# Kernel tuning notes

Hardware: AMD Instinct MI355X
Metric: run time of the kernel (lower is better)

Reference implementation:

```python
import jax, jax.numpy as jnp
import numpy as np

B, T, H, OUT_LEN, D_IN, D_OUT = 512, 512, 256, 8, 64, 64

def _lstm_seq(x, Wih, Whh, bih, bhh):
    # batch_first LSTM, zero initial state; x: [B,T,D] -> [B,T,H]
    b = bih + bhh
    h0 = jnp.zeros((x.shape[0], Whh.shape[1]), x.dtype)
    def step(carry, xt):
        h, c = carry
        g = xt @ Wih.T + h @ Whh.T + b
        i, f, gg, o = jnp.split(g, 4, axis=-1)  # torch gate order i,f,g,o
        c = jax.nn.sigmoid(f) * c + jax.nn.sigmoid(i) * jnp.tanh(gg)
        h = jax.nn.sigmoid(o) * jnp.tanh(c)
        return (h, c), h
    _, hs = jax.lax.scan(step, (h0, h0), jnp.swapaxes(x, 0, 1))
    return jnp.swapaxes(hs, 0, 1)

def _lstm_cell0(xt, Wih, bih, bhh):
    # single decode step; original calls self.dec with fresh zero (h,c) each
    # step, so the recurrent matrix Whh never contributes.
    g = xt @ Wih.T + bih + bhh
    i, f, gg, o = jnp.split(g, 4, axis=-1)
    c = jax.nn.sigmoid(i) * jnp.tanh(gg)
    return jax.nn.sigmoid(o) * jnp.tanh(c)

def _mlp(x, Ws, bs, Wl, bl):
    # simple.mlp: hidden Linear+ReLU stack, linear output (dropout off)
    for k in range(Ws.shape[0]):
        x = jax.nn.relu(x @ Ws[k] + bs[k])
    return x @ Wl + bl

def setup_inputs():
    key = jax.random.key(0)
    ks = iter(jax.random.split(key, 32))
    def W(shape, fan):
        return jax.random.normal(next(ks), shape, jnp.float32) / np.float32(np.sqrt(fan))
    return {
        'x': jax.random.normal(next(ks), (B, T, D_IN), jnp.float32),
        'in_W': W((D_IN, H), D_IN), 'in_b': jnp.zeros((H,), jnp.float32),
        'enc_Wih': W((4*H, H), H), 'enc_Whh': W((4*H, H), H),
        'enc_bih': jnp.zeros((4*H,), jnp.float32), 'enc_bhh': jnp.zeros((4*H,), jnp.float32),
        'dec_Wih': W((4*H, 2*H), 2*H), 'dec_Whh': W((4*H, H), H),
        'dec_bih': jnp.zeros((4*H,), jnp.float32), 'dec_bhh': jnp.zeros((4*H,), jnp.float32),
        'w_Ws': W((3, H, H), H), 'w_bs': jnp.zeros((3, H), jnp.float32), 'w_Wl': W((H, H), H), 'w_bl': jnp.zeros((H,), jnp.float32),
        'u_Ws': W((3, H, H), H), 'u_bs': jnp.zeros((3, H), jnp.float32), 'u_Wl': W((H, H), H), 'u_bl': jnp.zeros((H,), jnp.float32),
        'v_Ws': W((7, H, H), H), 'v_bs': jnp.zeros((7, H), jnp.float32), 'v_Wl': W((H, 1), H), 'v_bl': jnp.zeros((1,), jnp.float32),
        'out_W': W((H, D_OUT), H), 'out_b': jnp.zeros((D_OUT,), jnp.float32),
    }

def reference(x, in_W, in_b, enc_Wih, enc_Whh, enc_bih, enc_bhh,
              dec_Wih, dec_Whh, dec_bih, dec_bhh,
              w_Ws, w_bs, w_Wl, w_bl, u_Ws, u_bs, u_Wl, u_bl,
              v_Ws, v_bs, v_Wl, v_bl, out_W, out_b):
    h = x @ in_W + in_b                                       # input projection [B,T,H]
    enc = _lstm_seq(h, enc_Wih, enc_Whh, enc_bih, enc_bhh)    # [B,T,H]
    whs = _mlp(enc, w_Ws, w_bs, w_Wl, w_bl)                   # w(hs), loop-invariant (hoisted)
    def dec_step(s, _):
        us = _mlp(s, u_Ws, u_bs, u_Wl, u_bl)                  # [B,H]
        e = _mlp(jnp.tanh(us[:, None, :] + whs), v_Ws, v_bs, v_Wl, v_bl)  # [B,T,1]
        a = jax.nn.softmax(e, axis=1)                         # softmax over time
        c_t = jnp.sum(a * enc, axis=1)                        # [B,H] weighted sum
        s_new = _lstm_cell0(jnp.concatenate([c_t, s], axis=-1), dec_Wih, dec_bih, dec_bhh)
        return s_new, s_new
    s0 = jnp.zeros((x.shape[0], H), x.dtype)
    _, ss = jax.lax.scan(dec_step, s0, None, length=OUT_LEN)  # [OUT_LEN,B,H]
    dec = jnp.swapaxes(ss, 0, 1)                              # [B,OUT_LEN,H]
    return dec @ out_W + out_b                                # output projection
```

## Files before the change

kernel.cpp:

```cpp
#include <hip/hip_runtime.h>
#include <math.h>

#define B_    512
#define T_    512
#define H_    256
#define DIN_  64
#define OL_   8
#define DOUT_ 64

#define CBv   128
#define HSTR  32768

typedef unsigned short u16;
typedef unsigned int u32;
typedef unsigned long long ull;
typedef __attribute__((ext_vector_type(8))) short short8;
typedef __attribute__((ext_vector_type(4))) float f32x4;

static __device__ __forceinline__ float sigm(float x){ return 1.0f/(1.0f + expf(-x)); }
static __device__ __forceinline__ float bf2f(u16 h){
  u32 u = ((u32)h) << 16; float f; __builtin_memcpy(&f, &u, 4); return f;
}
static __device__ __forceinline__ u16 f2bf(float f){
  u32 u; __builtin_memcpy(&u, &f, 4);
  u = (u + 0x7fffu + ((u >> 16) & 1u)) >> 16;
  return (u16)u;
}
static __device__ __forceinline__ u32 packhl(float f){
  u16 h = f2bf(f);
  u16 lo = f2bf(f - bf2f(h));
  return ((u32)h << 16) | (u32)lo;
}
static __device__ __forceinline__ float unpackhl(u32 w){
  return bf2f((u16)(w >> 16)) + bf2f((u16)(w & 0xffff));
}
static __device__ __forceinline__ u32 al(const u32* p){
  return __hip_atomic_load(p, __ATOMIC_RELAXED, __HIP_MEMORY_SCOPE_AGENT);
}
static __device__ __forceinline__ void as_(u32* p, u32 v){
  __hip_atomic_store(p, v, __ATOMIC_RELAXED, __HIP_MEMORY_SCOPE_AGENT);
}

__global__ void k_wpt(const float* __restrict__ inW, const float* __restrict__ Wih,
                      float* __restrict__ WpT)
{
  int gid = blockIdx.x * 256 + threadIdx.x;
  int c = gid >> 6, d = gid & 63;
  const float* wr = Wih + c * H_;
  const float* ir = inW + d * H_;
  float acc = 0.f;
  #pragma unroll 4
  for (int e = 0; e < H_; e += 4) {
    float4 av = *(const float4*)(ir + e);
    float4 bv = *(const float4*)(wr + e);
    acc += av.x*bv.x + av.y*bv.y + av.z*bv.z + av.w*bv.w;
  }
  WpT[c*64 + d] = acc;
}

__global__ void k_bp(const float* __restrict__ inb, const float* __restrict__ Wih,
                     const float* __restrict__ bih, const float* __restrict__ bhh,
                     float* __restrict__ bp)
{
  int c = blockIdx.x * 256 + threadIdx.x;
  const float* wr = Wih + c * H_;
  float acc = bih[c] + bhh[c];
  for (int e = 0; e < H_; ++e) acc += inb[e] * wr[e];
  bp[c] = acc;
}

__global__ void k_dwt(const float* __restrict__ dWih, float* __restrict__ dWt)
{
  int gid = blockIdx.x * 256 + threadIdx.x;
  int j = gid >> 9, k = gid & 511;
  int row = (j < 256) ? j : (j + 256);
  dWt[k*768 + j] = dWih[row*512 + k];
}

__global__ void k_wall(const float* __restrict__ wWs, const float* __restrict__ wWl,
                       const float* __restrict__ uWs, const float* __restrict__ uWl,
                       const float* __restrict__ vWs, u16* __restrict__ outb)
{
  int lyr = blockIdx.y;
  const float* W = (lyr < 3)  ? wWs + lyr*65536
                 : (lyr == 3) ? wWl
                 : (lyr < 7)  ? uWs + (lyr-4)*65536
                 : (lyr == 7) ? uWl
                 :              vWs + (lyr-8)*65536;
  u16* out = outb + (size_t)lyr*131072;
  int gid = blockIdx.x * 256 + threadIdx.x;
  int k = gid & 255, n = gid >> 8;
  float v = W[k*256 + n];
  int s = k >> 5, j = k & 7;
  int lane = (((k >> 3) & 3) << 4) | (n & 15);
  int fl = ((s*16) + (n >> 4))*512 + lane*8 + j;
  u16 h = f2bf(v);
  out[fl] = h;
  out[65536 + fl] = f2bf(v - bf2f(h));
}

__global__ void k_whhfl(const float* __restrict__ Whh, u16* __restrict__ out)
{
  int gid = blockIdx.x * 256 + threadIdx.x;
  int j = gid & 7, l = (gid >> 3) & 63, ctg = (gid >> 9) & 63, s = gid >> 15;
  int k = s*32 + (l >> 4)*8 + j;
  int wv = ctg >> 2, g = ctg & 3;
  int row = g*256 + wv*16 + (l & 15);
  float v = Whh[row*256 + k];
  int fl = (s*64 + ctg)*512 + l*8 + j;
  u16 h = f2bf(v);
  out[fl] = h;
  out[262144 + fl] = f2bf(v - bf2f(h));
}

__global__ void k_wpfl(const float* __restrict__ WpT, u16* __restrict__ out)
{
  int gid = blockIdx.x * 256 + threadIdx.x;
  int j = gid & 7, l = (gid >> 3) & 63, ctg = (gid >> 9) & 63, s = gid >> 15;
  int k = s*32 + (l >> 4)*8 + j;
  int wv = ctg >> 2, g = ctg & 3;
  int row = g*256 + wv*16 + (l & 15);
  float v = WpT[row*64 + k];
  int fl = (s*64 + ctg)*512 + l*8 + j;
  u16 h = f2bf(v);
  out[fl] = h;
  out[65536 + fl] = f2bf(v - bf2f(h));
}

__global__ __launch_bounds__(256,1) void k_enc(
    const float* __restrict__ x, const u16* __restrict__ whhFL,
    const u16* __restrict__ wpFL, const float* __restrict__ bp,
    u32* __restrict__ henc)
{
  __shared__ float G[2][16][32][4];
  const int tid = threadIdx.x, l = tid & 63, wv = tid >> 6;
  const int lr = l & 15, lk = l >> 4;
  const int rg = blockIdx.x, bg = blockIdx.y, z = blockIdx.z;
  const int ug2 = wv >> 1;
  const int g0 = (wv & 1) * 2;
  const int u16g = bg*2 + ug2;

  short8 whH[8][2], whL[8][2], wpH[2][2], wpL[2][2];
  #pragma unroll
  for (int s = 0; s < 8; ++s)
    #pragma unroll
    for (int c = 0; c < 2; ++c) {
      int ctg = u16g*4 + g0 + c;
      whH[s][c] = *(const short8*)(whhFL + ((size_t)(s*64 + ctg))*512 + l*8);
      whL[s][c] = *(const short8*)(whhFL + 262144 + ((size_t)(s*64 + ctg))*512 + l*8);
    }
  #pragma unroll
  for (int s = 0; s < 2; ++s)
    #pragma unroll
    for (int c = 0; c < 2; ++c) {
      int ctg = u16g*4 + g0 + c;
      wpH[s][c] = *(const short8*)(wpFL + ((size_t)(s*64 + ctg))*512 + l*8);
      wpL[s][c] = *(const short8*)(wpFL + 65536 + ((size_t)(s*64 + ctg))*512 + l*8);
    }
  const int ul = tid & 31, er0 = tid >> 5;
  float bb[4];
  #pragma unroll
  for (int g = 0; g < 4; ++g) bb[g] = bp[g*256 + bg*32 + ul];
  float cs[2] = {0.f, 0.f};

  u32* hz = henc + (size_t)z * (size_t)(T_+1) * HSTR;
  const float* xrow = x + ((size_t)(z*CBv + rg*16 + lr)*T_)*DIN_ + lk*8;

  for (int t = 0; t < T_; ++t) {
    float4 xv0 = *(const float4*)(xrow);
    float4 xv1 = *(const float4*)(xrow + 4);
    float4 xv2 = *(const float4*)(xrow + 32);
    float4 xv3 = *(const float4*)(xrow + 36);
    xrow += DIN_;

    const ull* hb = (const ull*)(hz + (size_t)t*HSTR + (size_t)(rg*16 + lr)*256);
    ull hq[8][4];
    #pragma unroll
    for (int s = 0; s < 8; ++s)
      #pragma unroll
      for (int q = 0; q < 4; ++q)
        hq[s][q] = __hip_atomic_load(hb + s*16 + lk*4 + q,
                                     __ATOMIC_RELAXED, __HIP_MEMORY_SCOPE_AGENT);
    if (t) {
      for (;;) {
        bool ok = true;
        #pragma unroll
        for (int s = 0; s < 8; ++s)
          #pragma unroll
          for (int q = 0; q < 4; ++q) {
            u32 a = (u32)hq[s][q], b = (u32)(hq[s][q] >> 32);
            ok = ok && (a != 0u) && (b != 0u);
          }
        if (__all(ok)) break;
        __builtin_amdgcn_s_sleep(1);
        #pragma unroll
        for (int s = 0; s < 8; ++s)
          #pragma unroll
          for (int q = 0; q < 4; ++q)
            hq[s][q] = __hip_atomic_load(hb + s*16 + lk*4 + q,
                                         __ATOMIC_RELAXED, __HIP_MEMORY_SCOPE_AGENT);
      }
    }

    f32x4 acc[2];
    acc[0] = (f32x4){0.f,0.f,0.f,0.f};
    acc[1] = (f32x4){0.f,0.f,0.f,0.f};

    #pragma unroll
    for (int s = 0; s < 2; ++s) {
      float vv[8];
      if (s == 0) { vv[0]=xv0.x;vv[1]=xv0.y;vv[2]=xv0.z;vv[3]=xv0.w;vv[4]=xv1.x;vv[5]=xv1.y;vv[6]=xv1.z;vv[7]=xv1.w; }
      else        { vv[0]=xv2.x;vv[1]=xv2.y;vv[2]=xv2.z;vv[3]=xv2.w;vv[4]=xv3.x;vv[5]=xv3.y;vv[6]=xv3.z;vv[7]=xv3.w; }
      short8 ah, al2;
      #pragma unroll
      for (int j = 0; j < 8; ++j) {
        u16 h = f2bf(vv[j]);
        ah[j] = (short)h;
        al2[j] = (short)f2bf(vv[j] - bf2f(h));
      }
      #pragma unroll
      for (int c = 0; c < 2; ++c) {
        acc[c] = __builtin_amdgcn_mfma_f32_16x16x32_bf16(ah,  wpH[s][c], acc[c], 0,0,0);
        acc[c] = __builtin_amdgcn_mfma_f32_16x16x32_bf16(al2, wpH[s][c], acc[c], 0,0,0);
        acc[c] = __builtin_amdgcn_mfma_f32_16x16x32_bf16(ah,  wpL[s][c], acc[c], 0,0,0);
      }
    }
    #pragma unroll
    for (int s = 0; s < 8; ++s) {
      short8 ah, al2;
      #pragma unroll
      for (int q = 0; q < 4; ++q) {
        u32 w0 = (u32)hq[s][q], w1 = (u32)(hq[s][q] >> 32);
        ah[q*2]   = (short)(w0 >> 16); al2[q*2]   = (short)(w0 & 0xffff);
        ah[q*2+1] = (short)(w1 >> 16); al2[q*2+1] = (short)(w1 & 0xffff);
      }
      #pragma unroll
      for (int c = 0; c < 2; ++c) {
        acc[c] = __builtin_amdgcn_mfma_f32_16x16x32_bf16(ah,  whH[s][c], acc[c], 0,0,0);
        acc[c] = __builtin_amdgcn_mfma_f32_16x16x32_bf16(al2, whH[s][c], acc[c], 0,0,0);
        acc[c] = __builtin_amdgcn_mfma_f32_16x16x32_bf16(ah,  whL[s][c], acc[c], 0,0,0);
      }
    }

    const int p = t & 1;
    #pragma unroll
    for (int c = 0; c < 2; ++c)
      #pragma unroll
      for (int j = 0; j < 4; ++j)
        G[p][lk*4 + j][ug2*16 + lr][g0 + c] = acc[c][j];
    __syncthreads();

    #pragma unroll
    for (int pp = 0; pp < 2; ++pp) {
      int row = er0 + pp*8;
      float4 gq = *(const float4*)&G[p][row][ul][0];
      float gi = gq.x + bb[0], gf = gq.y + bb[1];
      float gg = gq.z + bb[2], go = gq.w + bb[3];
      float cn = sigm(gf)*cs[pp] + sigm(gi)*tanhf(gg);
      float hn = sigm(go)*tanhf(cn);
      cs[pp] = cn;
      as_(hz + (size_t)(t+1)*HSTR + (size_t)(rg*16 + row)*256 + bg*32 + ul,
          packhl(hn) | 1u);
    }
  }
}

static __device__ __forceinline__ void mlp_core(
    u32* act, const u16* wFL, const float* bs, const float* bl,
    int L, int nbs, bool lastRelu, int tid)
{
  const int l = tid & 63, cg = tid >> 6;
  const int lr = l & 15, lk = l >> 4;
  f32x4 acc[4][4];
  for (int lyr = 0; lyr < L; ++lyr) {
    __syncthreads();
    const u16* wb = wFL + (size_t)lyr*131072;
    #pragma unroll
    for (int rt = 0; rt < 4; ++rt)
      #pragma unroll
      for (int ct = 0; ct < 4; ++ct) acc[rt][ct] = (f32x4){0.f,0.f,0.f,0.f};

    short8 bh[2][4], blo[2][4];
    #pragma unroll
    for (int ct = 0; ct < 4; ++ct) {
      const u16* bfp = wb + ((size_t)(cg*4 + ct))*512 + l*8;
      bh[0][ct]  = *(const short8*)bfp;
      blo[0][ct] = *(const short8*)(bfp + 65536);
    }
    #pragma unroll
    for (int s = 0; s < 8; ++s) {
      const int pb = s & 1, nb = pb ^ 1;
      if (s < 7) {
        #pragma unroll
        for (int ct = 0; ct < 4; ++ct) {
          const u16* bfp = wb + ((size_t)((s+1)*16 + cg*4 + ct))*512 + l*8;
          bh[nb][ct]  = *(const short8*)bfp;
          blo[nb][ct] = *(const short8*)(bfp + 65536);
        }
      }
      short8 ah[4], al2[4];
      #pragma unroll
      for (int rt = 0; rt < 4; ++rt) {
        int row = rt*16 + lr;
        int cc = s*8 + lk*2;
        const u32* base = act + row*256;
        uint4 d0 = *(const uint4*)(base + (((cc    ) ^ (row & 7)) << 2));
        uint4 d1 = *(const uint4*)(base + (((cc + 1) ^ (row & 7)) << 2));
        u32 q[8] = {d0.x,d0.y,d0.z,d0.w,d1.x,d1.y,d1.z,d1.w};
        #pragma unroll
        for (int j = 0; j < 8; ++j) {
          ah[rt][j]  = (short)(q[j] >> 16);
          al2[rt][j] = (short)(q[j] & 0xffff);
        }
      }
      #pragma unroll
      for (int ct = 0; ct < 4; ++ct)
        #pragma unroll
        for (int rt = 0; rt < 4; ++rt) {
          acc[rt][ct] = __builtin_amdgcn_mfma_f32_16x16x32_bf16(ah[rt],  bh[pb][ct],  acc[rt][ct], 0,0,0);
          acc[rt][ct] = __builtin_amdgcn_mfma_f32_16x16x32_bf16(al2[rt], bh[pb][ct],  acc[rt][ct], 0,0,0);
          acc[rt][ct] = __builtin_amdgcn_mfma_f32_16x16x32_bf16(ah[rt],  blo[pb][ct], acc[rt][ct], 0,0,0);
        }
    }
    const float* bptr = (lyr < nbs) ? (bs + lyr*256) : bl;
    const bool dorelu = (lyr < L-1) || lastRelu;
    #pragma unroll
    for (int ct = 0; ct < 4; ++ct) {
      float bv = bptr[cg*64 + ct*16 + lr];
      #pragma unroll
      for (int rt = 0; rt < 4; ++rt)
        #pragma unroll
        for (int g = 0; g < 4; ++g) {
          float xv = acc[rt][ct][g] + bv;
          acc[rt][ct][g] = dorelu ? fmaxf(xv, 0.f) : xv;
        }
    }
    __syncthreads();
    #pragma unroll
    for (int ct = 0; ct < 4; ++ct) {
      int n = cg*64 + ct*16 + lr;
      #pragma unroll
      for (int rt = 0; rt < 4; ++rt)
        #pragma unroll
        for (int g = 0; g < 4; ++g) {
          int row = rt*16 + lk*4 + g;
          act[row*256 + (((n >> 2) ^ (row & 7)) << 2) + (n & 3)] = packhl(acc[rt][ct][g]);
        }
    }
  }
  __syncthreads();
}

__global__ __launch_bounds__(256,1) void k_dec_all(
    const u32* __restrict__ henc, const u16* __restrict__ mlpFL,
    const float* __restrict__ wbs, const float* __restrict__ wbl,
    const float* __restrict__ ubs, const float* __restrict__ ubl,
    const float* __restrict__ vbs, const float* __restrict__ vWl,
    const float* __restrict__ vbl,
    const float* __restrict__ dWt, const float* __restrict__ dbih,
    const float* __restrict__ dbhh,
    const float* __restrict__ oW, const float* __restrict__ ob,
    u32* __restrict__ whsP, u32* __restrict__ usb, u32* __restrict__ usflag,
    u32* __restrict__ eS, u32* __restrict__ ctxS, u32* __restrict__ sS,
    float* __restrict__ outc)
{
  extern __shared__ u32 act[];
  __shared__ float red[8];
  const int bid = blockIdx.x, tid = threadIdx.x;
  const u16* wFLw = mlpFL;
  const u16* wFLu = mlpFL + 4*131072;
  const u16* wFLv = mlpFL + 8*131072;
  float sprev[4] = {0.f, 0.f, 0.f, 0.f};

  for (int k = 0; k < 4; ++k) {
    long m0t = (long)(bid + 256*k) * 64;
    __syncthreads();
    for (int i = tid; i < 4096; i += 256) {
      int row = i >> 6, c16 = i & 63;
      long m = m0t + row;
      uint4 pk = *(const uint4*)(henc + HSTR + m*256 + c16*4);
      *((uint4*)(act + row*256 + ((c16 ^ (row & 7)) << 2))) = pk;
    }
    mlp_core(act, wFLw, wbs, wbl, 4, 3, false, tid);
    for (int i = tid; i < 4096; i += 256) {
      int row = i >> 6, c16 = i & 63;
      long m = m0t + row;
      uint4 pk = *((const uint4*)(act + row*256 + ((c16 ^ (row & 7)) << 2)));
      *(uint4*)(whsP + m*256 + c16*4) = pk;
    }
  }

  for (int s = 0; s < OL_; ++s) {
    if (bid < 2) {
      long m0t = (long)bid * 64;
      __syncthreads();
      for (int i = tid; i < 4096; i += 256) {
        int row = i >> 6, c16 = i & 63;
        const u32* sp = sS + (size_t)s*32768 + (m0t + row)*256 + c16*4;
        u32 w0 = al(sp), w1 = al(sp+1), w2 = al(sp+2), w3 = al(sp+3);
        if (s) {
          while (!(w0 && w1 && w2 && w3)) {
            __builtin_amdgcn_s_sleep(1);
            w0 = al(sp); w1 = al(sp+1); w2 = al(sp+2); w3 = al(sp+3);
          }
        }
        uint4 pk = { packhl(__uint_as_float(w0)), packhl(__uint_as_float(w1)),
                     packhl(__uint_as_float(w2)), packhl(__uint_as_float(w3)) };
        *((uint4*)(act + row*256 + ((c16 ^ (row & 7)) << 2))) = pk;
      }
      mlp_core(act, wFLu, ubs, ubl, 4, 3, false, tid);
      for (int i = tid; i < 4096; i += 256) {
        int row = i >> 6, c16 = i & 63;
        uint4 pk = *((const uint4*)(act + row*256 + ((c16 ^ (row & 7)) << 2)));
        *(uint4*)(usb + (size_t)s*32768 + (m0t + row)*256 + c16*4) = pk;
      }
      __syncthreads();
      if (tid == 0)
        __hip_atomic_store(usflag + s*2 + bid, 1u,
                           __ATOMIC_RELEASE, __HIP_MEMORY_SCOPE_AGENT);
    }

    {
      const u32* f0 = usflag + s*2;
      for (;;) {
        u32 a0 = al(f0), a1 = al(f0 + 1);
        if (a0 & a1) break;
        __builtin_amdgcn_s_sleep(2);
      }
      __builtin_amdgcn_fence(__ATOMIC_ACQUIRE, "agent");
    }

    for (int k = 0; k < 4; ++k) {
      long m0t = (long)(bid + 256*k) * 64;
      __syncthreads();
      for (int i = tid; i < 4096; i += 256) {
        int row = i >> 6, c16 = i & 63;
        long m = m0t + row;
        uint4 pw = *(const uint4*)(whsP + m*256 + c16*4);
        uint4 uw = *(const uint4*)(usb + (size_t)s*32768 + (m & 127)*256 + c16*4);
        uint4 pk;
        pk.x = packhl(tanhf(unpackhl(pw.x) + unpackhl(uw.x)));
        pk.y = packhl(tanhf(unpackhl(pw.y) + unpackhl(uw.y)));
        pk.z = packhl(tanhf(unpackhl(pw.z) + unpackhl(uw.z)));
        pk.w = packhl(tanhf(unpackhl(pw.w) + unpackhl(uw.w)));
        *((uint4*)(act + row*256 + ((c16 ^ (row & 7)) << 2))) = pk;
      }
      mlp_core(act, wFLv, vbs, vbs, 7, 7, true, tid);
      {
        int r2 = tid >> 2, q = tid & 3;
        float p = 0.f;
        #pragma unroll 8
        for (int j = 0; j < 64; ++j) {
          int n = q*64 + j;
          u32 w = act[r2*256 + (((n >> 2) ^ (r2 & 7)) << 2) + (n & 3)];
          p += unpackhl(w) * vWl[n];
        }
        p += __shfl_xor(p, 1, 64);
        p += __shfl_xor(p, 2, 64);
        if (q == 0)
          as_(eS + (size_t)s*65536 + m0t + r2, __float_as_uint(p + vbl[0]) | 1u);
      }
    }

    if (bid >= 64 && bid < 192) {
      int b = bid - 64;
      __syncthreads();
      float* asx = (float*)act;
      const u32* ep0 = eS + (size_t)s*65536 + b;
      u32 w0, w1;
      for (;;) {
        w0 = al(ep0 + (size_t)tid*128);
        w1 = al(ep0 + (size_t)(tid + 256)*128);
        if (w0 && w1) break;
        __builtin_amdgcn_s_sleep(1);
      }
      float v0 = __uint_as_float(w0), v1 = __uint_as_float(w1);
      const int lane = tid & 63, wv = tid >> 6;
      float m = fmaxf(v0, v1);
      #pragma unroll
      for (int o = 32; o; o >>= 1) m = fmaxf(m, __shfl_xor(m, o, 64));
      if (!lane) red[wv] = m;
      __syncthreads();
      m = fmaxf(fmaxf(red[0], red[1]), fmaxf(red[2], red[3]));
      float x0 = expf(v0 - m), x1 = expf(v1 - m);
      float sm = x0 + x1;
      #pragma unroll
      for (int o = 32; o; o >>= 1) sm += __shfl_xor(sm, o, 64);
      if (!lane) red[4 + wv] = sm;
      __syncthreads();
      float inv = 1.f / (red[4] + red[5] + red[6] + red[7]);
      asx[tid] = x0 * inv;
      asx[256 + tid] = x1 * inv;
      __syncthreads();
      float accv = 0.f;
      const u32* hp = henc + HSTR + (size_t)b*256 + tid;
      #pragma unroll 8
      for (int t = 0; t < 512; ++t) accv += asx[t] * unpackhl(hp[(size_t)t*HSTR]);
      as_(ctxS + (size_t)s*32768 + b*256 + tid, __float_as_uint(accv) | 1u);
    }

    if (bid >= 224) {
      int c = bid - 224, b0r = c*4;
      __syncthreads();
      float* xt = (float*)act;
      float cv[4];
      {
        const u32* cp = ctxS + (size_t)s*32768 + (size_t)b0r*256 + tid;
        u32 w0, w1, w2, w3;
        for (;;) {
          w0 = al(cp); w1 = al(cp + 256); w2 = al(cp + 512); w3 = al(cp + 768);
          if (w0 && w1 && w2 && w3) break;
          __builtin_amdgcn_s_sleep(1);
        }
        cv[0] = __uint_as_float(w0); cv[1] = __uint_as_float(w1);
        cv[2] = __uint_as_float(w2); cv[3] = __uint_as_float(w3);
      }
      #pragma unroll
      for (int bb = 0; bb < 4; ++bb) {
        xt[bb*520 + tid] = cv[bb];
        xt[bb*520 + 256 + tid] = sprev[bb];
      }
      __syncthreads();
      float ai[4], ag[4], ao[4];
      #pragma unroll
      for (int bb = 0; bb < 4; ++bb) { ai[bb]=0.f; ag[bb]=0.f; ao[bb]=0.f; }
      #pragma unroll 4
      for (int k = 0; k < 512; ++k) {
        float wi = dWt[k*768 + tid];
        float wg = dWt[k*768 + 256 + tid];
        float wo = dWt[k*768 + 512 + tid];
        #pragma unroll
        for (int bb = 0; bb < 4; ++bb) {
          float xv = xt[bb*520 + k];
          ai[bb] += xv*wi; ag[bb] += xv*wg; ao[bb] += xv*wo;
        }
      }
      float bi = dbih[tid]       + dbhh[tid];
      float bg = dbih[512 + tid] + dbhh[512 + tid];
      float bo = dbih[768 + tid] + dbhh[768 + tid];
      float snew[4];
      #pragma unroll
      for (int bb = 0; bb < 4; ++bb) {
        float cn = sigm(ai[bb] + bi) * tanhf(ag[bb] + bg);
        snew[bb] = sigm(ao[bb] + bo) * tanhf(cn);
        as_(sS + (size_t)(s+1)*32768 + (size_t)(b0r + bb)*256 + tid,
            __float_as_uint(snew[bb]) | 1u);
        sprev[bb] = snew[bb];
      }
      __syncthreads();
      float* sn = (float*)act;
      #pragma unroll
      for (int bb = 0; bb < 4; ++bb) sn[bb*256 + tid] = snew[bb];
      __syncthreads();
      int d = tid & 63, rr = tid >> 6;
      float a2 = ob[d];
      #pragma unroll 4
      for (int k = 0; k < 256; ++k) a2 += sn[rr*256 + k] * oW[k*64 + d];
      outc[((size_t)(b0r + rr)*OL_ + s)*64 + d] = a2;
    }
  }
}

extern "C" void kernel_launch(void* const* d_in, const int* in_sizes, int n_in,
                              void* d_out, int out_size, void* d_ws, size_t ws_size,
                              hipStream_t stream)
{
  (void)in_sizes; (void)n_in;
  const float* x    = (const float*)d_in[0];
  const float* inW  = (const float*)d_in[1];
  const float* inb  = (const float*)d_in[2];
  const float* eWih = (const float*)d_in[3];
  const float* eWhh = (const float*)d_in[4];
  const float* ebih = (const float*)d_in[5];
  const float* ebhh = (const float*)d_in[6];
  const float* dWih = (const float*)d_in[7];
  const float* dbih = (const float*)d_in[9];
  const float* dbhh = (const float*)d_in[10];
  const float* wWs  = (const float*)d_in[11];
  const float* wbs  = (const float*)d_in[12];
  const float* wWl  = (const float*)d_in[13];
  const float* wbl  = (const float*)d_in[14];
  const float* uWs  = (const float*)d_in[15];
  const float* ubs  = (const float*)d_in[16];
  const float* uWl  = (const float*)d_in[17];
  const float* ubl  = (const float*)d_in[18];
  const float* vWs  = (const float*)d_in[19];
  const float* vbs  = (const float*)d_in[20];
  const float* vWl  = (const float*)d_in[21];
  const float* vbl  = (const float*)d_in[22];
  const float* oW   = (const float*)d_in[23];
  const float* ob   = (const float*)d_in[24];
  float* out = (float*)d_out;

  hipFuncSetAttribute((const void*)k_dec_all, hipFuncAttributeMaxDynamicSharedMemorySize, 65536);

  const size_t hsz = (size_t)(T_+1) * HSTR;
  const size_t avail = ws_size / 4;
  auto needf = [&](int nc) -> size_t {
    return (size_t)nc*hsz + 16777216ull  + 1343552ull
         + 1770496ull  + 4096;
  };
  int NC = (needf(2) <= avail) ? 2 : 1;
  if (needf(NC) > avail) { hipMemsetAsync(d_out, 0, (size_t)out_size*4, stream); return; }

  float* wsf = (float*)d_ws;
  size_t o = 0;
  u32* henc = (u32*)(wsf + o);  o += (size_t)NC*hsz;
  u32* whsP = (u32*)(wsf + o);  o += 16777216;
  u32* usb  = (u32*)(wsf + o);  o += 262144;
  u32* usflag = (u32*)(wsf + o); o += 64;
  u32* eS   = (u32*)(wsf + o);  o += 524288;
  u32* ctxS = (u32*)(wsf + o);  o += 262144;
  u32* sS   = (u32*)(wsf + o);  o += 294912;
  float* WpT = wsf + o;  o += 65536;
  float* bp  = wsf + o;  o += 1024;
  float* dWt = wsf + o;  o += 393216;
  u16* whhFL = (u16*)(wsf + o);  o += 262144;
  u16* wpFL  = (u16*)(wsf + o);  o += 65536;
  u16* mlpFL = (u16*)(wsf + o);

  const size_t scratchBytes = (262144ull + 64 + 524288 + 262144 + 294912) * 4;

  k_wpt<<<256, 256, 0, stream>>>(inW, eWih, WpT);
  k_bp <<<4,   256, 0, stream>>>(inb, eWih, ebih, ebhh, bp);
  k_dwt<<<1536,256, 0, stream>>>(dWih, dWt);
  k_whhfl<<<1024,256,0,stream>>>(eWhh, whhFL);
  k_wpfl <<<256, 256,0,stream>>>(WpT, wpFL);
  k_wall <<<dim3(256,15), 256, 0, stream>>>(wWs, wWl, uWs, uWl, vWs, mlpFL);

  for (int c0 = 0; c0 < B_; c0 += CBv*NC) {
    hipMemsetAsync(henc, 0, (size_t)NC*hsz*4, stream);

    k_enc<<<dim3(CBv/16, 8, NC), 256, 0, stream>>>(
        x + (size_t)c0*T_*DIN_, whhFL, wpFL, bp, henc);

    for (int z = 0; z < NC; ++z) {
      hipMemsetAsync(usb, 0, scratchBytes, stream);
      k_dec_all<<<256, 256, 65536, stream>>>(
          henc + (size_t)z*hsz, mlpFL,
          wbs, wbl, ubs, ubl, vbs, vWl, vbl,
          dWt, dbih, dbhh, oW, ob,
          whsP, usb, usflag, eS, ctxS, sS,
          out + (size_t)(c0 + z*CBv)*OL_*DOUT_);
    }
  }
}
```

Before: 18.68 ms.

## Double decoder block size to 512 threads, splitting MLP rows and reductions

Launches the fused decoder kernel with 512 threads per block instead of 256. The MLP core now splits the 64-row tile across two row groups of waves, so each wave holds half the accumulators. The attention softmax, context sum, energy dot product and decoder LSTM cell all split their reductions across the extra threads, with shared-memory partial sums. The goal is more waves per CU to hide latency on the serial decode path. The cost is extra barriers and partial-sum traffic, and each wave now reloads the full weight tile, doubling weight fetches per block.

```diff
diff --git a/kernel.cpp b/kernel.cpp
--- a/kernel.cpp
+++ b/kernel.cpp
@@ -269,14 +269,16 @@
     u32* act, const u16* wFL, const float* bs, const float* bl,
     int L, int nbs, bool lastRelu, int tid)
 {
-  const int l = tid & 63, cg = tid >> 6;
+  const int l = tid & 63, w = tid >> 6;
+  const int rg = w >> 2, cg = w & 3;
   const int lr = l & 15, lk = l >> 4;
-  f32x4 acc[4][4];
+  const int wrow = rg*32;
+  f32x4 acc[2][4];
   for (int lyr = 0; lyr < L; ++lyr) {
     __syncthreads();
     const u16* wb = wFL + (size_t)lyr*131072;
     #pragma unroll
-    for (int rt = 0; rt < 4; ++rt)
+    for (int rt = 0; rt < 2; ++rt)
       #pragma unroll
       for (int ct = 0; ct < 4; ++ct) acc[rt][ct] = (f32x4){0.f,0.f,0.f,0.f};
 
@@ -298,10 +300,10 @@
           blo[nb][ct] = *(const short8*)(bfp + 65536);
         }
       }
-      short8 ah[4], al2[4];
-      #pragma unroll
-      for (int rt = 0; rt < 4; ++rt) {
-        int row = rt*16 + lr;
+      short8 ah[2], al2[2];
+      #pragma unroll
+      for (int rt = 0; rt < 2; ++rt) {
+        int row = wrow + rt*16 + lr;
         int cc = s*8 + lk*2;
         const u32* base = act + row*256;
         uint4 d0 = *(const uint4*)(base + (((cc    ) ^ (row & 7)) << 2));
@@ -316,7 +318,7 @@
       #pragma unroll
       for (int ct = 0; ct < 4; ++ct)
         #pragma unroll
-        for (int rt = 0; rt < 4; ++rt) {
+        for (int rt = 0; rt < 2; ++rt) {
           acc[rt][ct] = __builtin_amdgcn_mfma_f32_16x16x32_bf16(ah[rt],  bh[pb][ct],  acc[rt][ct], 0,0,0);
           acc[rt][ct] = __builtin_amdgcn_mfma_f32_16x16x32_bf16(al2[rt], bh[pb][ct],  acc[rt][ct], 0,0,0);
           acc[rt][ct] = __builtin_amdgcn_mfma_f32_16x16x32_bf16(ah[rt],  blo[pb][ct], acc[rt][ct], 0,0,0);
@@ -328,7 +330,7 @@
     for (int ct = 0; ct < 4; ++ct) {
       float bv = bptr[cg*64 + ct*16 + lr];
       #pragma unroll
-      for (int rt = 0; rt < 4; ++rt)
+      for (int rt = 0; rt < 2; ++rt)
         #pragma unroll
         for (int g = 0; g < 4; ++g) {
           float xv = acc[rt][ct][g] + bv;
@@ -340,10 +342,10 @@
     for (int ct = 0; ct < 4; ++ct) {
       int n = cg*64 + ct*16 + lr;
       #pragma unroll
-      for (int rt = 0; rt < 4; ++rt)
+      for (int rt = 0; rt < 2; ++rt)
         #pragma unroll
         for (int g = 0; g < 4; ++g) {
-          int row = rt*16 + lk*4 + g;
+          int row = wrow + rt*16 + lk*4 + g;
           act[row*256 + (((n >> 2) ^ (row & 7)) << 2) + (n & 3)] = packhl(acc[rt][ct][g]);
         }
     }
@@ -351,7 +353,7 @@
   __syncthreads();
 }
 
-__global__ __launch_bounds__(256,1) void k_dec_all(
+__global__ __launch_bounds__(512,1) void k_dec_all(
     const u32* __restrict__ henc, const u16* __restrict__ mlpFL,
     const float* __restrict__ wbs, const float* __restrict__ wbl,
     const float* __restrict__ ubs, const float* __restrict__ ubl,
@@ -365,7 +367,7 @@
     float* __restrict__ outc)
 {
   extern __shared__ u32 act[];
-  __shared__ float red[8];
+  __shared__ float red[8], red2[8];
   const int bid = blockIdx.x, tid = threadIdx.x;
   const u16* wFLw = mlpFL;
   const u16* wFLu = mlpFL + 4*131072;
@@ -375,14 +377,14 @@
   for (int k = 0; k < 4; ++k) {
     long m0t = (long)(bid + 256*k) * 64;
     __syncthreads();
-    for (int i = tid; i < 4096; i += 256) {
+    for (int i = tid; i < 4096; i += 512) {
       int row = i >> 6, c16 = i & 63;
       long m = m0t + row;
       uint4 pk = *(const uint4*)(henc + HSTR + m*256 + c16*4);
       *((uint4*)(act + row*256 + ((c16 ^ (row & 7)) << 2))) = pk;
     }
     mlp_core(act, wFLw, wbs, wbl, 4, 3, false, tid);
-    for (int i = tid; i < 4096; i += 256) {
+    for (int i = tid; i < 4096; i += 512) {
       int row = i >> 6, c16 = i & 63;
       long m = m0t + row;
       uint4 pk = *((const uint4*)(act + row*256 + ((c16 ^ (row & 7)) << 2)));
@@ -394,7 +396,7 @@
     if (bid < 2) {
       long m0t = (long)bid * 64;
       __syncthreads();
-      for (int i = tid; i < 4096; i += 256) {
+      for (int i = tid; i < 4096; i += 512) {
         int row = i >> 6, c16 = i & 63;
         const u32* sp = sS + (size_t)s*32768 + (m0t + row)*256 + c16*4;
         u32 w0 = al(sp), w1 = al(sp+1), w2 = al(sp+2), w3 = al(sp+3);
@@ -409,7 +411,7 @@
         *((uint4*)(act + row*256 + ((c16 ^ (row & 7)) << 2))) = pk;
       }
       mlp_core(act, wFLu, ubs, ubl, 4, 3, false, tid);
-      for (int i = tid; i < 4096; i += 256) {
+      for (int i = tid; i < 4096; i += 512) {
         int row = i >> 6, c16 = i & 63;
         uint4 pk = *((const uint4*)(act + row*256 + ((c16 ^ (row & 7)) << 2)));
         *(uint4*)(usb + (size_t)s*32768 + (m0t + row)*256 + c16*4) = pk;
@@ -421,19 +423,22 @@
     }
 
     {
-      const u32* f0 = usflag + s*2;
-      for (;;) {
-        u32 a0 = al(f0), a1 = al(f0 + 1);
-        if (a0 & a1) break;
-        __builtin_amdgcn_s_sleep(2);
-      }
+      if (tid < 64) {
+        const u32* f0 = usflag + s*2;
+        for (;;) {
+          u32 a0 = al(f0), a1 = al(f0 + 1);
+          if (a0 & a1) break;
+          __builtin_amdgcn_s_sleep(2);
+        }
+      }
+      __syncthreads();
       __builtin_amdgcn_fence(__ATOMIC_ACQUIRE, "agent");
     }
 
     for (int k = 0; k < 4; ++k) {
       long m0t = (long)(bid + 256*k) * 64;
       __syncthreads();
-      for (int i = tid; i < 4096; i += 256) {
+      for (int i = tid; i < 4096; i += 512) {
         int row = i >> 6, c16 = i & 63;
         long m = m0t + row;
         uint4 pw = *(const uint4*)(whsP + m*256 + c16*4);
@@ -447,16 +452,17 @@
       }
       mlp_core(act, wFLv, vbs, vbs, 7, 7, true, tid);
       {
-        int r2 = tid >> 2, q = tid & 3;
+        int r2 = tid >> 3, q = tid & 7;
         float p = 0.f;
         #pragma unroll 8
-        for (int j = 0; j < 64; ++j) {
-          int n = q*64 + j;
+        for (int j = 0; j < 32; ++j) {
+          int n = q*32 + j;
           u32 w = act[r2*256 + (((n >> 2) ^ (r2 & 7)) << 2) + (n & 3)];
           p += unpackhl(w) * vWl[n];
         }
         p += __shfl_xor(p, 1, 64);
         p += __shfl_xor(p, 2, 64);
+        p += __shfl_xor(p, 4, 64);
         if (q == 0)
           as_(eS + (size_t)s*65536 + m0t + r2, __float_as_uint(p + vbl[0]) | 1u);
       }
@@ -467,98 +473,119 @@
       __syncthreads();
       float* asx = (float*)act;
       const u32* ep0 = eS + (size_t)s*65536 + b;
-      u32 w0, w1;
+      u32 w0;
       for (;;) {
         w0 = al(ep0 + (size_t)tid*128);
-        w1 = al(ep0 + (size_t)(tid + 256)*128);
-        if (w0 && w1) break;
+        if (w0) break;
         __builtin_amdgcn_s_sleep(1);
       }
-      float v0 = __uint_as_float(w0), v1 = __uint_as_float(w1);
+      float v0 = __uint_as_float(w0);
       const int lane = tid & 63, wv = tid >> 6;
-      float m = fmaxf(v0, v1);
+      float m = v0;
       #pragma unroll
       for (int o = 32; o; o >>= 1) m = fmaxf(m, __shfl_xor(m, o, 64));
       if (!lane) red[wv] = m;
       __syncthreads();
-      m = fmaxf(fmaxf(red[0], red[1]), fmaxf(red[2], red[3]));
-      float x0 = expf(v0 - m), x1 = expf(v1 - m);
-      float sm = x0 + x1;
+      m = fmaxf(fmaxf(fmaxf(red[0], red[1]), fmaxf(red[2], red[3])),
+                fmaxf(fmaxf(red[4], red[5]), fmaxf(red[6], red[7])));
+      float x0 = expf(v0 - m);
+      float sm = x0;
       #pragma unroll
       for (int o = 32; o; o >>= 1) sm += __shfl_xor(sm, o, 64);
-      if (!lane) red[4 + wv] = sm;
-      __syncthreads();
-      float inv = 1.f / (red[4] + red[5] + red[6] + red[7]);
+      if (!lane) red2[wv] = sm;
+      __syncthreads();
+      float inv = 1.f / (red2[0] + red2[1] + red2[2] + red2[3]
+                       + red2[4] + red2[5] + red2[6] + red2[7]);
       asx[tid] = x0 * inv;
-      asx[256 + tid] = x1 * inv;
-      __syncthreads();
+      __syncthreads();
+      int unit = tid & 255, half = tid >> 8;
       float accv = 0.f;
-      const u32* hp = henc + HSTR + (size_t)b*256 + tid;
+      const u32* hp = henc + HSTR + (size_t)b*256 + unit;
       #pragma unroll 8
-      for (int t = 0; t < 512; ++t) accv += asx[t] * unpackhl(hp[(size_t)t*HSTR]);
-      as_(ctxS + (size_t)s*32768 + b*256 + tid, __float_as_uint(accv) | 1u);
+      for (int t = half*256; t < half*256 + 256; ++t)
+        accv += asx[t] * unpackhl(hp[(size_t)t*HSTR]);
+      float* part = asx + 512;
+      part[tid] = accv;
+      __syncthreads();
+      if (half == 0)
+        as_(ctxS + (size_t)s*32768 + b*256 + unit,
+            __float_as_uint(accv + part[256 + unit]) | 1u);
     }
 
     if (bid >= 224) {
       int c = bid - 224, b0r = c*4;
       __syncthreads();
       float* xt = (float*)act;
-      float cv[4];
-      {
-        const u32* cp = ctxS + (size_t)s*32768 + (size_t)b0r*256 + tid;
+      const int u = tid & 255, kh = tid >> 8;
+      if (kh == 0) {
+        const u32* cp = ctxS + (size_t)s*32768 + (size_t)b0r*256 + u;
         u32 w0, w1, w2, w3;
         for (;;) {
           w0 = al(cp); w1 = al(cp + 256); w2 = al(cp + 512); w3 = al(cp + 768);
           if (w0 && w1 && w2 && w3) break;
           __builtin_amdgcn_s_sleep(1);
         }
-        cv[0] = __uint_as_float(w0); cv[1] = __uint_as_float(w1);
-        cv[2] = __uint_as_float(w2); cv[3] = __uint_as_float(w3);
-      }
-      #pragma unroll
-      for (int bb = 0; bb < 4; ++bb) {
-        xt[bb*520 + tid] = cv[bb];
-        xt[bb*520 + 256 + tid] = sprev[bb];
+        xt[0*520 + u] = __uint_as_float(w0);
+        xt[1*520 + u] = __uint_as_float(w1);
+        xt[2*520 + u] = __uint_as_float(w2);
+        xt[3*520 + u] = __uint_as_float(w3);
+        #pragma unroll
+        for (int bb = 0; bb < 4; ++bb) xt[bb*520 + 256 + u] = sprev[bb];
       }
       __syncthreads();
       float ai[4], ag[4], ao[4];
       #pragma unroll
       for (int bb = 0; bb < 4; ++bb) { ai[bb]=0.f; ag[bb]=0.f; ao[bb]=0.f; }
       #pragma unroll 4
-      for (int k = 0; k < 512; ++k) {
-        float wi = dWt[k*768 + tid];
-        float wg = dWt[k*768 + 256 + tid];
-        float wo = dWt[k*768 + 512 + tid];
+      for (int k = kh*256; k < kh*256 + 256; ++k) {
+        float wi = dWt[k*768 + u];
+        float wg = dWt[k*768 + 256 + u];
+        float wo = dWt[k*768 + 512 + u];
         #pragma unroll
         for (int bb = 0; bb < 4; ++bb) {
           float xv = xt[bb*520 + k];
           ai[bb] += xv*wi; ag[bb] += xv*wg; ao[bb] += xv*wo;
         }
       }
-      float bi = dbih[tid]       + dbhh[tid];
-      float bg = dbih[512 + tid] + dbhh[512 + tid];
-      float bo = dbih[768 + tid] + dbhh[768 + tid];
-      float snew[4];
-      #pragma unroll
-      for (int bb = 0; bb < 4; ++bb) {
-        float cn = sigm(ai[bb] + bi) * tanhf(ag[bb] + bg);
-        snew[bb] = sigm(ao[bb] + bo) * tanhf(cn);
-        as_(sS + (size_t)(s+1)*32768 + (size_t)(b0r + bb)*256 + tid,
-            __float_as_uint(snew[bb]) | 1u);
-        sprev[bb] = snew[bb];
-      }
-      __syncthreads();
-      float* sn = (float*)act;
-      #pragma unroll
-      for (int bb = 0; bb < 4; ++bb) sn[bb*256 + tid] = snew[bb];
-      __syncthreads();
-      int d = tid & 63, rr = tid >> 6;
-      float a2 = ob[d];
-      #pragma unroll 4
-      for (int k = 0; k < 256; ++k) a2 += sn[rr*256 + k] * oW[k*64 + d];
-      outc[((size_t)(b0r + rr)*OL_ + s)*64 + d] = a2;
+      float* pr = xt + 4*520;
+      if (kh) {
+        #pragma unroll
+        for (int bb = 0; bb < 4; ++bb) {
+          pr[(0*4 + bb)*256 + u] = ai[bb];
+          pr[(1*4 + bb)*256 + u] = ag[bb];
+          pr[(2*4 + bb)*256 + u] = ao[bb];
+        }
+      }
+      __syncthreads();
+      float* sn = pr + 3*4*256;
+      if (!kh) {
+        float bi = dbih[u]       + dbhh[u];
+        float bg = dbih[512 + u] + dbhh[512 + u];
+        float bo = dbih[768 + u] + dbhh[768 + u];
+        #pragma unroll
+        for (int bb = 0; bb < 4; ++bb) {
+          float a1 = ai[bb] + pr[(0*4 + bb)*256 + u];
+          float g1 = ag[bb] + pr[(1*4 + bb)*256 + u];
+          float o1 = ao[bb] + pr[(2*4 + bb)*256 + u];
+          float cn = sigm(a1 + bi) * tanhf(g1 + bg);
+          float hn = sigm(o1 + bo) * tanhf(cn);
+          as_(sS + (size_t)(s+1)*32768 + (size_t)(b0r + bb)*256 + u,
+              __float_as_uint(hn) | 1u);
+          sprev[bb] = hn;
+          sn[bb*256 + u] = hn;
+        }
+      }
+      __syncthreads();
+      if (tid < 256) {
+        int d = tid & 63, rr = tid >> 6;
+        float a2 = ob[d];
+        #pragma unroll 4
+        for (int k = 0; k < 256; ++k) a2 += sn[rr*256 + k] * oW[k*64 + d];
+        outc[((size_t)(b0r + rr)*OL_ + s)*64 + d] = a2;
+      }
     }
   }
+  (void)wFLw;
 }
 
 extern "C" void kernel_launch(void* const* d_in, const int* in_sizes, int n_in,
@@ -636,7 +663,7 @@
 
     for (int z = 0; z < NC; ++z) {
       hipMemsetAsync(usb, 0, scratchBytes, stream);
-      k_dec_all<<<256, 256, 65536, stream>>>(
+      k_dec_all<<<256, 512, 65536, stream>>>(
           henc + (size_t)z*hsz, mlpFL,
           wbs, wbl, ubs, ubl, vbs, vWl, vbl,
           dWt, dbih, dbhh, oW, ob,
```

New measurement: 18.63 ms. No clear change (-0.3%).
